# Performance work log

Hardware: AMD Instinct MI355X
Metric: run time of the kernel (lower is better)

Reference implementation:

```python
import jax, jax.numpy as jnp
import numpy as np

B, L, D, H = 4, 2048, 1024, 16
DH = D // H

def setup_inputs() -> dict:
    key = jax.random.key(0)
    k1, k2, k3 = jax.random.split(key, 3)
    x = jax.random.normal(k1, (B, L, D), dtype=jnp.float32)
    w_qkv = jax.random.normal(k2, (3 * D, D), dtype=jnp.float32) * (1.0 / np.sqrt(D))
    w_proj = jax.random.normal(k3, (D, D), dtype=jnp.float32) * (1.0 / np.sqrt(D))
    return {"x": x, "w_qkv": w_qkv, "w_proj": w_proj}

def reference(x, w_qkv, w_proj):
    b, l, d = x.shape
    scale = 1.0 / np.sqrt(DH)
    qkv = (x @ w_qkv.T).reshape(b, l, 3, H, DH)
    qkv = jnp.transpose(qkv, (2, 0, 3, 1, 4))
    q, k, v = qkv[0], qkv[1], qkv[2]
    scores = jnp.einsum('bhqd,bhkd->bhqk', q, k) * scale
    attn = jax.nn.softmax(scores, axis=-1)
    out = jnp.einsum('bhqk,bhkd->bhqd', attn, v)
    out = jnp.transpose(out, (0, 2, 1, 3)).reshape(b, l, d)
    return out @ w_proj.T
```

## Files before the change

kernel.cpp:

```cpp
#include <hip/hip_runtime.h>
#include <hip/hip_bf16.h>


typedef __bf16  bf16x8  __attribute__((ext_vector_type(8)));
typedef __bf16  bf16x4  __attribute__((ext_vector_type(4)));
typedef float   floatx4 __attribute__((ext_vector_type(4)));

__device__ __forceinline__ void async_ld16(const void* g, void* lds_base_uniform) {
  __builtin_amdgcn_global_load_lds(
      (const __attribute__((address_space(1))) void*)g,
      (__attribute__((address_space(3))) void*)lds_base_uniform,
      16, 0, 0);
}

__device__ __forceinline__ int detect_bf16(const void* p) {
  const unsigned short* u = (const unsigned short*)p;
  int sane = 0;
#pragma unroll 4
  for (int i = 0; i < 64; ++i) {
    unsigned short w = u[2 * i];
    int e = (w >> 7) & 0xFF;
    sane += (w == 0 || (e >= 100 && e <= 150)) ? 1 : 0;
  }
  return sane >= 32;
}

__device__ __forceinline__ bf16x8 ld8_f32cvt(const void* base, size_t elem) {
  const float* p = (const float*)base + elem;
  floatx4 u0 = *(const floatx4*)p;
  floatx4 u1 = *(const floatx4*)(p + 4);
  bf16x8 v;
  v[0] = (__bf16)u0[0]; v[1] = (__bf16)u0[1]; v[2] = (__bf16)u0[2]; v[3] = (__bf16)u0[3];
  v[4] = (__bf16)u1[0]; v[5] = (__bf16)u1[1]; v[6] = (__bf16)u1[2]; v[7] = (__bf16)u1[3];
  return v;
}

template<int CTRL>
__device__ __forceinline__ float dpp_f(float x) {
  return __builtin_bit_cast(float,
      __builtin_amdgcn_update_dpp(0, __builtin_bit_cast(int, x), CTRL, 0xF, 0xF, true));
}
__device__ __forceinline__ float row16_sum(float x) {
  x += dpp_f<0xB1>(x);
  x += dpp_f<0x4E>(x);
  x += dpp_f<0x141>(x);
  x += dpp_f<0x140>(x);
  return x;
}

__launch_bounds__(256)
__global__ void cvt3_kernel(const void* __restrict__ s0, __bf16* __restrict__ d0, int n0,
                            const void* __restrict__ s1, __bf16* __restrict__ d1, int n1,
                            const void* __restrict__ s2, __bf16* __restrict__ d2) {
  int u = blockIdx.x * blockDim.x + threadIdx.x;
  const void* src; __bf16* dst;
  if (u < n0)           { src = s0; dst = d0; }
  else if (u < n0 + n1) { src = s1; dst = d1; u -= n0; }
  else                  { src = s2; dst = d2; u -= n0 + n1; }
  const int is_bf16 = detect_bf16(src);
  const size_t e = (size_t)u * 8;
  if (is_bf16) *(bf16x8*)(dst + e) = *(const bf16x8*)((const __bf16*)src + e);
  else         *(bf16x8*)(dst + e) = ld8_f32cvt(src, e);
}

template<int EPI>
__launch_bounds__(256, 2)
__global__ void gemm_bt_kernel(const __bf16* __restrict__ A,
                               const __bf16* __restrict__ B,
                               const void* __restrict__ oprobe,
                               void* __restrict__ Cout,
                               __bf16* __restrict__ qb,
                               __bf16* __restrict__ kb,
                               __bf16* __restrict__ vtb,
                               int M, int N, int K)
{
  __shared__ __align__(16) __bf16 As[128 * 32];
  __shared__ __align__(16) __bf16 Bs[128 * 32];

  const int flat = blockIdx.x;
  const int m0 = (((flat & 7) << 3) | ((flat >> 3) & 7)) << 7;
  const int n0 = (flat >> 6) << 7;

  const int tid  = threadIdx.x;
  const int wave = tid >> 6;
  const int lane = tid & 63;
  const int quad = lane >> 4;
  const int l16  = lane & 15;
  const int wm   = wave >> 1;
  const int wn   = wave & 1;

  const int r_in   = lane >> 2;
  const int cchunk = lane & 3;

  const __bf16* Ab = A + (size_t)m0 * K;
  const __bf16* Bb = B + (size_t)n0 * K;

  floatx4 acc[4][4];
#pragma unroll
  for (int i = 0; i < 4; ++i)
#pragma unroll
    for (int j = 0; j < 4; ++j)
      acc[i][j] = (floatx4){0.f, 0.f, 0.f, 0.f};

  const int ca0 = wave * 2;
  for (int k0 = 0; k0 < K; k0 += 32) {
#pragma unroll
    for (int i = 0; i < 2; ++i) {
      const int ca  = ca0 + i;
      const int row = ca * 16 + r_in;
      async_ld16(Ab + (size_t)row * K + k0 + cchunk * 8, (char*)As + ca * 1024);
      async_ld16(Bb + (size_t)row * K + k0 + cchunk * 8, (char*)Bs + ca * 1024);
    }
    __syncthreads();

    bf16x8 af[4], bfr[4];
#pragma unroll
    for (int tt = 0; tt < 4; ++tt) {
      af[tt]  = *(const bf16x8*)&As[(wm * 64 + tt * 16 + l16) * 32 + quad * 8];
      bfr[tt] = *(const bf16x8*)&Bs[(wn * 64 + tt * 16 + l16) * 32 + quad * 8];
    }
#pragma unroll
    for (int mt = 0; mt < 4; ++mt)
#pragma unroll
      for (int nt = 0; nt < 4; ++nt)
        acc[mt][nt] = __builtin_amdgcn_mfma_f32_16x16x32_bf16(af[mt], bfr[nt], acc[mt][nt], 0, 0, 0);
    __syncthreads();
  }

  const int out_bf16 = (EPI == 1) ? detect_bf16(oprobe) : 0;

#pragma unroll
  for (int mt = 0; mt < 4; ++mt) {
#pragma unroll
    for (int nt = 0; nt < 4; ++nt) {
      const int n_idx = n0 + wn * 64 + nt * 16 + l16;
      const int mbase = m0 + wm * 64 + mt * 16 + quad * 4;
      if (EPI == 1) {
        if (out_bf16) {
#pragma unroll
          for (int r = 0; r < 4; ++r)
            ((__bf16*)Cout)[(size_t)(mbase + r) * N + n_idx] = (__bf16)acc[mt][nt][r];
        } else {
#pragma unroll
          for (int r = 0; r < 4; ++r)
            ((float*)Cout)[(size_t)(mbase + r) * N + n_idx] = acc[mt][nt][r];
        }
      } else {
        const int sel = n_idx >> 10;
        const int rem = n_idx & 1023;
        const int h   = rem >> 6;
        const int dh  = rem & 63;
        const int b   = mbase >> 11;
        const int l   = mbase & 2047;
        const int bh  = b * 16 + h;
        if (sel == 2) {
          bf16x4 pk;
#pragma unroll
          for (int r = 0; r < 4; ++r) pk[r] = (__bf16)acc[mt][nt][r];
          *(bf16x4*)&vtb[((size_t)bh * 64 + dh) * 2048 + l] = pk;
        } else {
          __bf16* dstb = (sel == 0 ? qb : kb) + ((size_t)bh * 2048 + l) * 64 + dh;
#pragma unroll
          for (int r = 0; r < 4; ++r)
            dstb[(size_t)r * 64] = (__bf16)acc[mt][nt][r];
        }
      }
    }
  }
}

__launch_bounds__(256, 4)
__global__ void attn_kernel(const __bf16* __restrict__ qb,
                            const __bf16* __restrict__ kb,
                            const __bf16* __restrict__ vtb,
                            __bf16* __restrict__ ob )
{
  __shared__ __align__(16) __bf16 Ks[64 * 72];
  __shared__ __align__(16) __bf16 Vs[80 * 72];
  __shared__ __align__(16) __bf16 Ps[4][32 * 72];

  const int tid  = threadIdx.x;
  const int wave = tid >> 6;
  const int lane = tid & 63;
  const int quad = lane >> 4;
  const int l16  = lane & 15;

  const int bh = blockIdx.y;
  const int q0 = blockIdx.x * 128;

  const __bf16* Qp = qb  + (size_t)bh * 2048 * 64;
  const __bf16* Kp = kb  + (size_t)bh * 2048 * 64;
  const __bf16* Vp = vtb + (size_t)bh * 64 * 2048;

  for (int i = tid; i < 16 * 72; i += 256)
    Vs[64 * 72 + i] = (i < 72) ? (__bf16)1.0f : (__bf16)0.0f;

  const float C1 = 0.125f * 1.44269504f;
  const float C2 = -8.0f  * 1.44269504f;

  bf16x8 aq[2][2];
#pragma unroll
  for (int rt = 0; rt < 2; ++rt) {
    const __bf16* qrow = Qp + (size_t)(q0 + wave * 32 + rt * 16 + l16) * 64;
    aq[rt][0] = *(const bf16x8*)(qrow + quad * 8);
    aq[rt][1] = *(const bf16x8*)(qrow + 32 + quad * 8);
  }

  floatx4 o[2][4], o5[2];
#pragma unroll
  for (int rt = 0; rt < 2; ++rt) {
    o5[rt] = (floatx4){0.f, 0.f, 0.f, 0.f};
#pragma unroll
    for (int dt = 0; dt < 4; ++dt) o[rt][dt] = (floatx4){0.f, 0.f, 0.f, 0.f};
  }

  const int srow0 = tid >> 3;
  const int scc   = (tid & 7) * 8;

  {
#pragma unroll
    for (int it = 0; it < 2; ++it) {
      const int row = srow0 + it * 32;
      *(bf16x8*)&Ks[row * 72 + scc] = *(const bf16x8*)(Kp + (size_t)row * 64 + scc);
      *(bf16x8*)&Vs[row * 72 + scc] = *(const bf16x8*)(Vp + (size_t)row * 2048 + scc);
    }
  }
  __syncthreads();

  for (int kt = 0; kt < 32; ++kt) {
    const int kn = (((kt + 1) & 31) << 6);
    bf16x8 kreg[2], vreg[2];
#pragma unroll
    for (int it = 0; it < 2; ++it) {
      const int row = srow0 + it * 32;
      kreg[it] = *(const bf16x8*)(Kp + (size_t)(kn + row) * 64 + scc);
      vreg[it] = *(const bf16x8*)(Vp + (size_t)row * 2048 + kn + scc);
    }

    floatx4 st[2][4];
#pragma unroll
    for (int nt = 0; nt < 4; ++nt) {
      const int krow = nt * 16 + l16;
      bf16x8 ak0 = *(const bf16x8*)&Ks[krow * 72 + quad * 8];
      bf16x8 ak1 = *(const bf16x8*)&Ks[krow * 72 + 32 + quad * 8];
#pragma unroll
      for (int rt = 0; rt < 2; ++rt) {
        floatx4 z = (floatx4){0.f, 0.f, 0.f, 0.f};
        z = __builtin_amdgcn_mfma_f32_16x16x32_bf16(ak0, aq[rt][0], z, 0, 0, 0);
        z = __builtin_amdgcn_mfma_f32_16x16x32_bf16(ak1, aq[rt][1], z, 0, 0, 0);
        st[rt][nt] = z;
      }
    }

#pragma unroll
    for (int rt = 0; rt < 2; ++rt) {
#pragma unroll
      for (int nt = 0; nt < 4; ++nt) {
        bf16x4 pk;
#pragma unroll
        for (int r = 0; r < 4; ++r)
          pk[r] = (__bf16)__builtin_amdgcn_exp2f(fmaf(st[rt][nt][r], C1, C2));
        *(bf16x4*)&Ps[wave][(rt * 16 + l16) * 72 + nt * 16 + quad * 4] = pk;
      }
    }

    __builtin_amdgcn_wave_barrier();

    bf16x8 ap[2][2];
#pragma unroll
    for (int rt = 0; rt < 2; ++rt) {
      ap[rt][0] = *(const bf16x8*)&Ps[wave][(rt * 16 + l16) * 72 + quad * 8];
      ap[rt][1] = *(const bf16x8*)&Ps[wave][(rt * 16 + l16) * 72 + 32 + quad * 8];
    }

#pragma unroll
    for (int dt = 0; dt < 4; ++dt) {
      const int vrow = dt * 16 + l16;
      bf16x8 bv0 = *(const bf16x8*)&Vs[vrow * 72 + quad * 8];
      bf16x8 bv1 = *(const bf16x8*)&Vs[vrow * 72 + 32 + quad * 8];
#pragma unroll
      for (int rt = 0; rt < 2; ++rt) {
        o[rt][dt] = __builtin_amdgcn_mfma_f32_16x16x32_bf16(ap[rt][0], bv0, o[rt][dt], 0, 0, 0);
        o[rt][dt] = __builtin_amdgcn_mfma_f32_16x16x32_bf16(ap[rt][1], bv1, o[rt][dt], 0, 0, 0);
      }
    }
    {
      const int vrow = 64 + l16;
      bf16x8 bv0 = *(const bf16x8*)&Vs[vrow * 72 + quad * 8];
      bf16x8 bv1 = *(const bf16x8*)&Vs[vrow * 72 + 32 + quad * 8];
#pragma unroll
      for (int rt = 0; rt < 2; ++rt) {
        o5[rt] = __builtin_amdgcn_mfma_f32_16x16x32_bf16(ap[rt][0], bv0, o5[rt], 0, 0, 0);
        o5[rt] = __builtin_amdgcn_mfma_f32_16x16x32_bf16(ap[rt][1], bv1, o5[rt], 0, 0, 0);
      }
    }

    __syncthreads();
#pragma unroll
    for (int it = 0; it < 2; ++it) {
      const int row = srow0 + it * 32;
      *(bf16x8*)&Ks[row * 72 + scc] = kreg[it];
      *(bf16x8*)&Vs[row * 72 + scc] = vreg[it];
    }
    __syncthreads();
  }

  const int b = bh >> 4;
  const int h = bh & 15;
#pragma unroll
  for (int rt = 0; rt < 2; ++rt)
#pragma unroll
    for (int r = 0; r < 4; ++r) {
      const float lv  = row16_sum(l16 == 0 ? o5[rt][r] : 0.f);
      const float inv = 1.f / lv;
      const size_t rowbase =
          ((size_t)b * 2048 + q0 + wave * 32 + rt * 16 + quad * 4 + r) * 1024 + h * 64;
#pragma unroll
      for (int dt = 0; dt < 4; ++dt)
        ob[rowbase + dt * 16 + l16] = (__bf16)(o[rt][dt][r] * inv);
    }
}

extern "C" void kernel_launch(void* const* d_in, const int* in_sizes, int n_in,
                              void* d_out, int out_size, void* d_ws, size_t ws_size,
                              hipStream_t stream)
{
  (void)in_sizes; (void)n_in; (void)out_size; (void)ws_size;

  const void* x     = d_in[0];
  const void* wqkv  = d_in[1];
  const void* wproj = d_in[2];

  const size_t NX    = (size_t)8192 * 1024;
  const size_t NWQKV = (size_t)3072 * 1024;
  const size_t NWPRJ = (size_t)1024 * 1024;

  __bf16* qbuf   = (__bf16*)d_ws;
  __bf16* kbuf   = qbuf + NX;
  __bf16* vtbuf  = kbuf + NX;
  __bf16* abuf   = vtbuf + NX;
  __bf16* xb     = abuf + NX;
  __bf16* wqkvb  = xb + NX;
  __bf16* wprojb = wqkvb + NWQKV;

  dim3 blk(256);

  cvt3_kernel<<<dim3((NX + NWQKV + NWPRJ) / 2048), blk, 0, stream>>>(
      x, xb, NX / 8, wqkv, wqkvb, NWQKV / 8, wproj, wprojb);

  gemm_bt_kernel<0><<<dim3(24 * 64), blk, 0, stream>>>(
      xb, wqkvb, nullptr, nullptr, qbuf, kbuf, vtbuf, 8192, 3072, 1024);

  attn_kernel<<<dim3(2048 / 128, 64), blk, 0, stream>>>(qbuf, kbuf, vtbuf, abuf);

  gemm_bt_kernel<1><<<dim3(8 * 64), blk, 0, stream>>>(
      abuf, wprojb, wproj, d_out, nullptr, nullptr, nullptr, 8192, 1024, 1024);
}
```

Baseline: 290.3 us.

## Keep softmax probabilities in registers and double-buffer K/V tiles in attention

The attention kernel stops staging the exponentiated scores through per-wave LDS. It instead feeds them straight from registers into 16x16x16 bf16 MFMAs, whose A-operand layout matches the score accumulator layout. K/V shared tiles are double-buffered, which removes one __syncthreads per iteration, and the ones-row used for the row-sum comes from a register constant instead of extra LDS rows. The cost is twice as many, smaller MFMA instructions for P·V and the row-sum, and more LDS for the second buffer.

```diff
diff --git a/kernel.cpp b/kernel.cpp
--- a/kernel.cpp
+++ b/kernel.cpp
@@ -5,12 +5,22 @@
 typedef __bf16  bf16x8  __attribute__((ext_vector_type(8)));
 typedef __bf16  bf16x4  __attribute__((ext_vector_type(4)));
 typedef float   floatx4 __attribute__((ext_vector_type(4)));
+typedef short   s16x4   __attribute__((ext_vector_type(4)));
 
 __device__ __forceinline__ void async_ld16(const void* g, void* lds_base_uniform) {
   __builtin_amdgcn_global_load_lds(
       (const __attribute__((address_space(1))) void*)g,
       (__attribute__((address_space(3))) void*)lds_base_uniform,
       16, 0, 0);
+}
+
+__device__ __forceinline__ floatx4 mfma16(s16x4 a, s16x4 b, floatx4 c) {
+#if __has_builtin(__builtin_amdgcn_mfma_f32_16x16x16bf16_1k)
+  return __builtin_amdgcn_mfma_f32_16x16x16bf16_1k(a, b, c, 0, 0, 0);
+#else
+  asm("v_mfma_f32_16x16x16_bf16 %0, %1, %2, %0" : "+v"(c) : "v"(a), "v"(b));
+  return c;
+#endif
 }
 
 __device__ __forceinline__ int detect_bf16(const void* p) {
@@ -175,9 +185,8 @@
                             const __bf16* __restrict__ vtb,
                             __bf16* __restrict__ ob )
 {
-  __shared__ __align__(16) __bf16 Ks[64 * 72];
-  __shared__ __align__(16) __bf16 Vs[80 * 72];
-  __shared__ __align__(16) __bf16 Ps[4][32 * 72];
+  __shared__ __align__(16) __bf16 Ks[2][64 * 72];
+  __shared__ __align__(16) __bf16 Vs[2][64 * 72];
 
   const int tid  = threadIdx.x;
   const int wave = tid >> 6;
@@ -192,9 +201,6 @@
   const __bf16* Kp = kb  + (size_t)bh * 2048 * 64;
   const __bf16* Vp = vtb + (size_t)bh * 64 * 2048;
 
-  for (int i = tid; i < 16 * 72; i += 256)
-    Vs[64 * 72 + i] = (i < 72) ? (__bf16)1.0f : (__bf16)0.0f;
-
   const float C1 = 0.125f * 1.44269504f;
   const float C2 = -8.0f  * 1.44269504f;
 
@@ -206,6 +212,14 @@
     aq[rt][1] = *(const bf16x8*)(qrow + 32 + quad * 8);
   }
 
+  s16x4 bvo;
+  {
+    bf16x4 onev;
+    const __bf16 ov = (l16 == 0) ? (__bf16)1.0f : (__bf16)0.0f;
+    onev[0] = ov; onev[1] = ov; onev[2] = ov; onev[3] = ov;
+    bvo = __builtin_bit_cast(s16x4, onev);
+  }
+
   floatx4 o[2][4], o5[2];
 #pragma unroll
   for (int rt = 0; rt < 2; ++rt) {
@@ -217,17 +231,17 @@
   const int srow0 = tid >> 3;
   const int scc   = (tid & 7) * 8;
 
-  {
-#pragma unroll
-    for (int it = 0; it < 2; ++it) {
-      const int row = srow0 + it * 32;
-      *(bf16x8*)&Ks[row * 72 + scc] = *(const bf16x8*)(Kp + (size_t)row * 64 + scc);
-      *(bf16x8*)&Vs[row * 72 + scc] = *(const bf16x8*)(Vp + (size_t)row * 2048 + scc);
-    }
+#pragma unroll
+  for (int it = 0; it < 2; ++it) {
+    const int row = srow0 + it * 32;
+    *(bf16x8*)&Ks[0][row * 72 + scc] = *(const bf16x8*)(Kp + (size_t)row * 64 + scc);
+    *(bf16x8*)&Vs[0][row * 72 + scc] = *(const bf16x8*)(Vp + (size_t)row * 2048 + scc);
   }
   __syncthreads();
 
   for (int kt = 0; kt < 32; ++kt) {
+    const int cur = kt & 1;
+    const int nxt = cur ^ 1;
     const int kn = (((kt + 1) & 31) << 6);
     bf16x8 kreg[2], vreg[2];
 #pragma unroll
@@ -237,12 +251,15 @@
       vreg[it] = *(const bf16x8*)(Vp + (size_t)row * 2048 + kn + scc);
     }
 
+    const __bf16* Kc = &Ks[cur][0];
+    const __bf16* Vc = &Vs[cur][0];
+
     floatx4 st[2][4];
 #pragma unroll
     for (int nt = 0; nt < 4; ++nt) {
       const int krow = nt * 16 + l16;
-      bf16x8 ak0 = *(const bf16x8*)&Ks[krow * 72 + quad * 8];
-      bf16x8 ak1 = *(const bf16x8*)&Ks[krow * 72 + 32 + quad * 8];
+      bf16x8 ak0 = *(const bf16x8*)&Kc[krow * 72 + quad * 8];
+      bf16x8 ak1 = *(const bf16x8*)&Kc[krow * 72 + 32 + quad * 8];
 #pragma unroll
       for (int rt = 0; rt < 2; ++rt) {
         floatx4 z = (floatx4){0.f, 0.f, 0.f, 0.f};
@@ -252,55 +269,43 @@
       }
     }
 
+    s16x4 pa[2][4];
 #pragma unroll
     for (int rt = 0; rt < 2; ++rt) {
 #pragma unroll
       for (int nt = 0; nt < 4; ++nt) {
-        bf16x4 pk;
+        bf16x4 p;
 #pragma unroll
         for (int r = 0; r < 4; ++r)
-          pk[r] = (__bf16)__builtin_amdgcn_exp2f(fmaf(st[rt][nt][r], C1, C2));
-        *(bf16x4*)&Ps[wave][(rt * 16 + l16) * 72 + nt * 16 + quad * 4] = pk;
+          p[r] = (__bf16)__builtin_amdgcn_exp2f(fmaf(st[rt][nt][r], C1, C2));
+        pa[rt][nt] = __builtin_bit_cast(s16x4, p);
       }
     }
 
-    __builtin_amdgcn_wave_barrier();
-
-    bf16x8 ap[2][2];
-#pragma unroll
-    for (int rt = 0; rt < 2; ++rt) {
-      ap[rt][0] = *(const bf16x8*)&Ps[wave][(rt * 16 + l16) * 72 + quad * 8];
-      ap[rt][1] = *(const bf16x8*)&Ps[wave][(rt * 16 + l16) * 72 + 32 + quad * 8];
-    }
-
 #pragma unroll
     for (int dt = 0; dt < 4; ++dt) {
-      const int vrow = dt * 16 + l16;
-      bf16x8 bv0 = *(const bf16x8*)&Vs[vrow * 72 + quad * 8];
-      bf16x8 bv1 = *(const bf16x8*)&Vs[vrow * 72 + 32 + quad * 8];
-#pragma unroll
-      for (int rt = 0; rt < 2; ++rt) {
-        o[rt][dt] = __builtin_amdgcn_mfma_f32_16x16x32_bf16(ap[rt][0], bv0, o[rt][dt], 0, 0, 0);
-        o[rt][dt] = __builtin_amdgcn_mfma_f32_16x16x32_bf16(ap[rt][1], bv1, o[rt][dt], 0, 0, 0);
-      }
-    }
-    {
-      const int vrow = 64 + l16;
-      bf16x8 bv0 = *(const bf16x8*)&Vs[vrow * 72 + quad * 8];
-      bf16x8 bv1 = *(const bf16x8*)&Vs[vrow * 72 + 32 + quad * 8];
-#pragma unroll
-      for (int rt = 0; rt < 2; ++rt) {
-        o5[rt] = __builtin_amdgcn_mfma_f32_16x16x32_bf16(ap[rt][0], bv0, o5[rt], 0, 0, 0);
-        o5[rt] = __builtin_amdgcn_mfma_f32_16x16x32_bf16(ap[rt][1], bv1, o5[rt], 0, 0, 0);
-      }
-    }
-
-    __syncthreads();
+      const __bf16* vr = &Vc[(dt * 16 + l16) * 72];
+      s16x4 vb[4];
+#pragma unroll
+      for (int nt = 0; nt < 4; ++nt)
+        vb[nt] = __builtin_bit_cast(s16x4, *(const bf16x4*)&vr[nt * 16 + quad * 4]);
+#pragma unroll
+      for (int nt = 0; nt < 4; ++nt)
+#pragma unroll
+        for (int rt = 0; rt < 2; ++rt)
+          o[rt][dt] = mfma16(pa[rt][nt], vb[nt], o[rt][dt]);
+    }
+#pragma unroll
+    for (int nt = 0; nt < 4; ++nt)
+#pragma unroll
+      for (int rt = 0; rt < 2; ++rt)
+        o5[rt] = mfma16(pa[rt][nt], bvo, o5[rt]);
+
 #pragma unroll
     for (int it = 0; it < 2; ++it) {
       const int row = srow0 + it * 32;
-      *(bf16x8*)&Ks[row * 72 + scc] = kreg[it];
-      *(bf16x8*)&Vs[row * 72 + scc] = vreg[it];
+      *(bf16x8*)&Ks[nxt][row * 72 + scc] = kreg[it];
+      *(bf16x8*)&Vs[nxt][row * 72 + scc] = vreg[it];
     }
     __syncthreads();
   }
```

Result: slower. 307.7 us (+6.0%).

## Double-buffer K/V in LDS with per-wave load split and single barrier

Applied to the files above, without the earlier changes.

Replaces the separate K, V and P shared arrays with two K/V buffers. Each wave's softmax P tile aliases the slice of the next buffer that this same wave will later fill with prefetched data, which removes one of the two block-wide barriers per key tile. K loads go to waves 0-1 and V loads to waves 2-3. The row-sum ones row now lives in registers instead of LDS, and s_setprio is raised around the MFMA blocks. The aliasing depends on each wave writing only its own P region, so the indexing must match exactly; the change also brings a small reduction in LDS footprint.

```diff
diff --git a/kernel.cpp b/kernel.cpp
--- a/kernel.cpp
+++ b/kernel.cpp
@@ -175,9 +175,7 @@
                             const __bf16* __restrict__ vtb,
                             __bf16* __restrict__ ob )
 {
-  __shared__ __align__(16) __bf16 Ks[64 * 72];
-  __shared__ __align__(16) __bf16 Vs[80 * 72];
-  __shared__ __align__(16) __bf16 Ps[4][32 * 72];
+  __shared__ __align__(16) __bf16 S[2][2 * 64 * 72];
 
   const int tid  = threadIdx.x;
   const int wave = tid >> 6;
@@ -192,9 +190,6 @@
   const __bf16* Kp = kb  + (size_t)bh * 2048 * 64;
   const __bf16* Vp = vtb + (size_t)bh * 64 * 2048;
 
-  for (int i = tid; i < 16 * 72; i += 256)
-    Vs[64 * 72 + i] = (i < 72) ? (__bf16)1.0f : (__bf16)0.0f;
-
   const float C1 = 0.125f * 1.44269504f;
   const float C2 = -8.0f  * 1.44269504f;
 
@@ -206,6 +201,13 @@
     aq[rt][1] = *(const bf16x8*)(qrow + 32 + quad * 8);
   }
 
+  bf16x8 onesb;
+  {
+    const __bf16 ov = (l16 == 0) ? (__bf16)1.0f : (__bf16)0.0f;
+#pragma unroll
+    for (int i = 0; i < 8; ++i) onesb[i] = ov;
+  }
+
   floatx4 o[2][4], o5[2];
 #pragma unroll
   for (int rt = 0; rt < 2; ++rt) {
@@ -214,35 +216,60 @@
     for (int dt = 0; dt < 4; ++dt) o[rt][dt] = (floatx4){0.f, 0.f, 0.f, 0.f};
   }
 
-  const int srow0 = tid >> 3;
-  const int scc   = (tid & 7) * 8;
+  const int sarr = wave >> 1;
+  const int srb  = (wave & 1) * 32;
+  const int sr0  = lane >> 3;
+  const int scol = (lane & 7) * 8;
 
   {
-#pragma unroll
-    for (int it = 0; it < 2; ++it) {
-      const int row = srow0 + it * 32;
-      *(bf16x8*)&Ks[row * 72 + scc] = *(const bf16x8*)(Kp + (size_t)row * 64 + scc);
-      *(bf16x8*)&Vs[row * 72 + scc] = *(const bf16x8*)(Vp + (size_t)row * 2048 + scc);
+    __bf16* dst = &S[0][sarr * (64 * 72)];
+    if (sarr == 0) {
+#pragma unroll
+      for (int i = 0; i < 4; ++i) {
+        const int row = srb + sr0 + 8 * i;
+        *(bf16x8*)&dst[row * 72 + scol] = *(const bf16x8*)(Kp + (size_t)row * 64 + scol);
+      }
+    } else {
+#pragma unroll
+      for (int i = 0; i < 4; ++i) {
+        const int row = srb + sr0 + 8 * i;
+        *(bf16x8*)&dst[row * 72 + scol] = *(const bf16x8*)(Vp + (size_t)row * 2048 + scol);
+      }
     }
   }
   __syncthreads();
 
   for (int kt = 0; kt < 32; ++kt) {
-    const int kn = (((kt + 1) & 31) << 6);
-    bf16x8 kreg[2], vreg[2];
-#pragma unroll
-    for (int it = 0; it < 2; ++it) {
-      const int row = srow0 + it * 32;
-      kreg[it] = *(const bf16x8*)(Kp + (size_t)(kn + row) * 64 + scc);
-      vreg[it] = *(const bf16x8*)(Vp + (size_t)row * 2048 + kn + scc);
-    }
+    const int cur = kt & 1;
+    const int nxt = cur ^ 1;
+    const int kn  = (((kt + 1) & 31) << 6);
+
+    bf16x8 sreg[4];
+    if (sarr == 0) {
+#pragma unroll
+      for (int i = 0; i < 4; ++i) {
+        const int row = srb + sr0 + 8 * i;
+        sreg[i] = *(const bf16x8*)(Kp + (size_t)(kn + row) * 64 + scol);
+      }
+    } else {
+#pragma unroll
+      for (int i = 0; i < 4; ++i) {
+        const int row = srb + sr0 + 8 * i;
+        sreg[i] = *(const bf16x8*)(Vp + (size_t)row * 2048 + kn + scol);
+      }
+    }
+
+    const __bf16* Kc = &S[cur][0];
+    const __bf16* Vc = &S[cur][64 * 72];
+    __bf16*       Pq = &S[nxt][0] + wave * 2304;
 
     floatx4 st[2][4];
+    __builtin_amdgcn_s_setprio(1);
 #pragma unroll
     for (int nt = 0; nt < 4; ++nt) {
       const int krow = nt * 16 + l16;
-      bf16x8 ak0 = *(const bf16x8*)&Ks[krow * 72 + quad * 8];
-      bf16x8 ak1 = *(const bf16x8*)&Ks[krow * 72 + 32 + quad * 8];
+      bf16x8 ak0 = *(const bf16x8*)&Kc[krow * 72 + quad * 8];
+      bf16x8 ak1 = *(const bf16x8*)&Kc[krow * 72 + 32 + quad * 8];
 #pragma unroll
       for (int rt = 0; rt < 2; ++rt) {
         floatx4 z = (floatx4){0.f, 0.f, 0.f, 0.f};
@@ -251,6 +278,7 @@
         st[rt][nt] = z;
       }
     }
+    __builtin_amdgcn_s_setprio(0);
 
 #pragma unroll
     for (int rt = 0; rt < 2; ++rt) {
@@ -260,7 +288,7 @@
 #pragma unroll
         for (int r = 0; r < 4; ++r)
           pk[r] = (__bf16)__builtin_amdgcn_exp2f(fmaf(st[rt][nt][r], C1, C2));
-        *(bf16x4*)&Ps[wave][(rt * 16 + l16) * 72 + nt * 16 + quad * 4] = pk;
+        *(bf16x4*)&Pq[(rt * 16 + l16) * 72 + nt * 16 + quad * 4] = pk;
       }
     }
 
@@ -269,38 +297,38 @@
     bf16x8 ap[2][2];
 #pragma unroll
     for (int rt = 0; rt < 2; ++rt) {
-      ap[rt][0] = *(const bf16x8*)&Ps[wave][(rt * 16 + l16) * 72 + quad * 8];
-      ap[rt][1] = *(const bf16x8*)&Ps[wave][(rt * 16 + l16) * 72 + 32 + quad * 8];
-    }
-
+      ap[rt][0] = *(const bf16x8*)&Pq[(rt * 16 + l16) * 72 + quad * 8];
+      ap[rt][1] = *(const bf16x8*)&Pq[(rt * 16 + l16) * 72 + 32 + quad * 8];
+    }
+
+    __builtin_amdgcn_s_setprio(1);
 #pragma unroll
     for (int dt = 0; dt < 4; ++dt) {
       const int vrow = dt * 16 + l16;
-      bf16x8 bv0 = *(const bf16x8*)&Vs[vrow * 72 + quad * 8];
-      bf16x8 bv1 = *(const bf16x8*)&Vs[vrow * 72 + 32 + quad * 8];
+      bf16x8 bv0 = *(const bf16x8*)&Vc[vrow * 72 + quad * 8];
+      bf16x8 bv1 = *(const bf16x8*)&Vc[vrow * 72 + 32 + quad * 8];
 #pragma unroll
       for (int rt = 0; rt < 2; ++rt) {
         o[rt][dt] = __builtin_amdgcn_mfma_f32_16x16x32_bf16(ap[rt][0], bv0, o[rt][dt], 0, 0, 0);
         o[rt][dt] = __builtin_amdgcn_mfma_f32_16x16x32_bf16(ap[rt][1], bv1, o[rt][dt], 0, 0, 0);
       }
     }
+#pragma unroll
+    for (int rt = 0; rt < 2; ++rt) {
+      o5[rt] = __builtin_amdgcn_mfma_f32_16x16x32_bf16(ap[rt][0], onesb, o5[rt], 0, 0, 0);
+      o5[rt] = __builtin_amdgcn_mfma_f32_16x16x32_bf16(ap[rt][1], onesb, o5[rt], 0, 0, 0);
+    }
+    __builtin_amdgcn_s_setprio(0);
+
+    __builtin_amdgcn_wave_barrier();
+
     {
-      const int vrow = 64 + l16;
-      bf16x8 bv0 = *(const bf16x8*)&Vs[vrow * 72 + quad * 8];
-      bf16x8 bv1 = *(const bf16x8*)&Vs[vrow * 72 + 32 + quad * 8];
-#pragma unroll
-      for (int rt = 0; rt < 2; ++rt) {
-        o5[rt] = __builtin_amdgcn_mfma_f32_16x16x32_bf16(ap[rt][0], bv0, o5[rt], 0, 0, 0);
-        o5[rt] = __builtin_amdgcn_mfma_f32_16x16x32_bf16(ap[rt][1], bv1, o5[rt], 0, 0, 0);
-      }
-    }
-
-    __syncthreads();
-#pragma unroll
-    for (int it = 0; it < 2; ++it) {
-      const int row = srow0 + it * 32;
-      *(bf16x8*)&Ks[row * 72 + scc] = kreg[it];
-      *(bf16x8*)&Vs[row * 72 + scc] = vreg[it];
+      __bf16* dst = &S[nxt][sarr * (64 * 72)];
+#pragma unroll
+      for (int i = 0; i < 4; ++i) {
+        const int row = srb + sr0 + 8 * i;
+        *(bf16x8*)&dst[row * 72 + scol] = sreg[i];
+      }
     }
     __syncthreads();
   }
```

After: 283.2 us. -2.4%, faster.
